# Kernel tuning notes

Hardware: AMD Instinct MI355X
Metric: run time of the kernel (lower is better)

## Reference

```python
import jax, jax.numpy as jnp
import numpy as np

MIN_C = 1e-6
MIN_NORM = 1e-15
BALL_EPS = 0.004  # float32 ball epsilon


def _norm(x):
    return jnp.maximum(jnp.linalg.norm(x, axis=-1, keepdims=True), MIN_NORM)


def _project(x, c):
    norm = _norm(x)
    maxnorm = (1.0 - BALL_EPS) / jnp.sqrt(c)
    return jnp.where(norm > maxnorm, x / norm * maxnorm, x)


def _tanh(x):
    return jnp.tanh(jnp.clip(x, -15.0, 15.0))


def _artanh(x):
    x = jnp.clip(x, -1.0 + 1e-5, 1.0 - 1e-5)
    return 0.5 * (jnp.log1p(x) - jnp.log1p(-x))


def _expmap0(u, c):
    sc = jnp.sqrt(c)
    n = _norm(u)
    return _project(_tanh(sc * n) * u / (sc * n), c)


def _logmap0(y, c):
    sc = jnp.sqrt(c)
    n = _norm(y)
    return y / n / sc * _artanh(sc * n)


def _mobius_add(x, y, c):
    x2 = jnp.sum(x * x, -1, keepdims=True)
    y2 = jnp.sum(y * y, -1, keepdims=True)
    xy = jnp.sum(x * y, -1, keepdims=True)
    num = (1 + 2 * c * xy + c * y2) * x + (1 - c * x2) * y
    den = jnp.maximum(1 + 2 * c * xy + c * c * x2 * y2, MIN_NORM)
    return num / den


N_NODE, N_EDGE, D, ATTN, B, N_VOCAB = 100000, 1000000, 64, 64, 256, 401


def setup_inputs() -> dict:
    key = jax.random.key(0)
    ks = jax.random.split(key, 12)
    r_idx = jax.random.randint(ks[0], (N_EDGE,), 0, B, dtype=jnp.int32)
    rel = jax.random.randint(ks[1], (N_EDGE,), 0, N_VOCAB, dtype=jnp.int32)
    sub = jax.random.randint(ks[2], (N_EDGE,), 0, N_NODE, dtype=jnp.int32)
    obj = jax.random.randint(ks[3], (N_EDGE,), 0, N_NODE, dtype=jnp.int32)
    zero = jnp.zeros((N_EDGE,), jnp.int32)
    edges = jnp.stack([r_idx, zero, rel, zero, sub, obj], axis=1)  # [E, 6]
    s = 0.1
    return {
        "hidden": jax.random.normal(ks[4], (N_NODE, D), jnp.float32) * s,
        "q_rel": jax.random.randint(ks[5], (B,), 0, N_VOCAB, dtype=jnp.int32),
        "edges": edges,
        "rela_embed": jax.random.normal(ks[6], (N_VOCAB, D), jnp.float32) * s,
        "Ws_w": jax.random.normal(ks[7], (ATTN, D), jnp.float32) * s,
        "Wr_w": jax.random.normal(ks[8], (ATTN, D), jnp.float32) * s,
        "Wqr_w": jax.random.normal(ks[9], (ATTN, D), jnp.float32) * s,
        "Wqr_b": jnp.zeros((ATTN,), jnp.float32),
        "Wattn_w": jax.random.normal(ks[10], (1, ATTN), jnp.float32) * s,
        "Wh_w": jax.random.normal(ks[11], (D, D), jnp.float32) * s,
        "n_node": N_NODE,
    }


def reference(hidden, q_rel, edges, rela_embed, Ws_w, Wr_w, Wqr_w, Wqr_b, Wattn_w, Wh_w, n_node):
    c = MIN_C
    sub, rel, obj, r_idx = edges[:, 4], edges[:, 2], edges[:, 5], edges[:, 0]
    hs = hidden[sub]                 # [E, D] gather
    hr = rela_embed[rel]             # [E, D]
    h_qr = rela_embed[q_rel][r_idx]  # [E, D]
    # attention MLP -> scalar gate per edge
    pre = hs @ Ws_w.T + hr @ Wr_w.T + h_qr @ Wqr_w.T + Wqr_b
    alpha = jax.nn.sigmoid(jax.nn.relu(pre) @ Wattn_w.T)  # [E, 1]
    # hyperbolic message
    hs_h = _expmap0(hs, c)
    hr_h = _expmap0(hr, c)
    mess2 = _logmap0(_project(_mobius_add(hs_h, hr_h, c), c), c)
    message = mess2 * alpha
    agg = jax.ops.segment_sum(message, obj, num_segments=n_node)  # scatter-add
    a = _expmap0(agg @ Wh_w.T, c)
    a = jax.nn.relu(a)  # act
    return _logmap0(a, c)
```

## Files before the change

### kernel.cpp

```cpp
#include <hip/hip_runtime.h>
#include <math.h>
#include <stdint.h>

#define N_NODE 100000
#define N_EDGE 1000000
#define DIM    64
#define NB     256
#define NVOCAB 401
#define AGG_WAVES 8192
#define NSTREAM (AGG_WAVES * 4)

#define BSH    9
#define BMSK   511
#define NBKT   ((N_NODE + BMSK) >> BSH)
#define CHKE   1024
#define NCHK   ((N_EDGE + CHKE - 1) / CHKE)
#define SCAN_TOT (NBKT * NCHK)
#define SCANA_GRID ((SCAN_TOT + 1023) / 1024)

typedef short short8  __attribute__((ext_vector_type(8)));
typedef float floatx4 __attribute__((ext_vector_type(4)));
typedef unsigned short ushort_t;

__device__ inline unsigned short f2bf_rne(float f)
{
    unsigned u = __float_as_uint(f);
    unsigned r = u + 0x7FFF + ((u >> 16) & 1);
    return (unsigned short)(r >> 16);
}
__device__ inline float bflo(unsigned u) { return __uint_as_float(u << 16); }
__device__ inline float bfhi(unsigned u) { return __uint_as_float(u & 0xFFFF0000u); }
__device__ inline unsigned short f2h(float f)
{
    _Float16 h = (_Float16)f;
    unsigned short s; __builtin_memcpy(&s, &h, 2); return s;
}
__device__ inline float h2f(unsigned b)
{
    unsigned short s = (unsigned short)b;
    _Float16 h; __builtin_memcpy(&h, &s, 2); return (float)h;
}

__device__ inline void split8(float4 v0, float4 v1, short8& hi, short8& lo)
{
    float f[8] = {v0.x, v0.y, v0.z, v0.w, v1.x, v1.y, v1.z, v1.w};
    #pragma unroll
    for (int j = 0; j < 8; ++j) {
        unsigned u = __float_as_uint(f[j]);
        unsigned r = u + 0x7FFF + ((u >> 16) & 1);
        unsigned short h = (unsigned short)(r >> 16);
        float hf = __uint_as_float(((unsigned)h) << 16);
        float l  = f[j] - hf;
        unsigned u2 = __float_as_uint(l);
        unsigned r2 = u2 + 0x7FFF + ((u2 >> 16) & 1);
        hi[j] = (short)h;
        lo[j] = (short)(r2 >> 16);
    }
}

#define INIT_GRID ((4 * 4096 + 255) / 256)

__global__ __launch_bounds__(256) void init_kernel(
    const float* __restrict__ Ws, const float* __restrict__ Wr,
    const float* __restrict__ Wqr, const float* __restrict__ Wh,
    ushort_t* __restrict__ wsp)
{
    int tid = blockIdx.x * 256 + threadIdx.x;
    if (tid < 4 * 4096) {
        int w = tid >> 12, e = tid & 4095;
        const float* src = (w == 0) ? Ws : (w == 1) ? Wr : (w == 2) ? Wqr : Wh;
        float f = src[e];
        unsigned u = __float_as_uint(f);
        unsigned r = u + 0x7FFF + ((u >> 16) & 1);
        unsigned short h = (unsigned short)(r >> 16);
        float hf = __uint_as_float(((unsigned)h) << 16);
        float l  = f - hf;
        unsigned u2 = __float_as_uint(l);
        unsigned r2 = u2 + 0x7FFF + ((u2 >> 16) & 1);
        wsp[w * 8192 + e]        = h;
        wsp[w * 8192 + 4096 + e] = (unsigned short)(r2 >> 16);
    }
}

__device__ void gemm64p_body(
    const float* __restrict__ X,
    const int*   __restrict__ idx,
    const ushort_t* __restrict__ Whi,
    const ushort_t* __restrict__ Wlo,
    const float* __restrict__ bias,
    void* __restrict__ Yv,
    ushort_t* __restrict__ Y2,
    int R, int out_mode, int blk)
{
    int wave = threadIdx.x >> 6;
    int lane = threadIdx.x & 63;
    int m    = lane & 15;
    int quad = lane >> 4;
    int r0   = blk * 64 + wave * 16;

    int r = r0 + m;
    int src = (r < R) ? (idx ? idx[r] : r) : 0;
    const float* xrow = X + (size_t)src * DIM + quad * 8;

    float4 a0[2], a1[2];
    #pragma unroll
    for (int c = 0; c < 2; ++c) {
        a0[c] = *(const float4*)(xrow + 32 * c);
        a1[c] = *(const float4*)(xrow + 32 * c + 4);
    }
    short8 ah[2], al[2];
    #pragma unroll
    for (int c = 0; c < 2; ++c) split8(a0[c], a1[c], ah[c], al[c]);

    if (out_mode == 3 && r < R) {
        #pragma unroll
        for (int c = 0; c < 2; ++c)
            *(short8*)(Y2 + (size_t)r * DIM + 32 * c + quad * 8) = ah[c];
    }

    floatx4 acc[4] = {{0,0,0,0},{0,0,0,0},{0,0,0,0},{0,0,0,0}};
    #pragma unroll
    for (int g = 0; g < 4; ++g) {
        const ushort_t* whrow = Whi + (size_t)(g * 16 + m) * DIM + quad * 8;
        const ushort_t* wlrow = Wlo + (size_t)(g * 16 + m) * DIM + quad * 8;
        #pragma unroll
        for (int c = 0; c < 2; ++c) {
            short8 bh = *(const short8*)(whrow + 32 * c);
            short8 bl = *(const short8*)(wlrow + 32 * c);
            acc[g] = __builtin_amdgcn_mfma_f32_16x16x32_bf16(bh, ah[c], acc[g], 0, 0, 0);
            acc[g] = __builtin_amdgcn_mfma_f32_16x16x32_bf16(bl, ah[c], acc[g], 0, 0, 0);
            acc[g] = __builtin_amdgcn_mfma_f32_16x16x32_bf16(bh, al[c], acc[g], 0, 0, 0);
        }
    }

    if (r < R) {
        #pragma unroll
        for (int g = 0; g < 4; ++g) {
            float4 bv = make_float4(0.f, 0.f, 0.f, 0.f);
            if (bias) bv = *(const float4*)(bias + g * 16 + quad * 4);
            float v0 = acc[g][0] + bv.x;
            float v1 = acc[g][1] + bv.y;
            float v2 = acc[g][2] + bv.z;
            float v3 = acc[g][3] + bv.w;
            if (out_mode == 1) {
                v0 = fmaxf(v0, 0.f); v1 = fmaxf(v1, 0.f);
                v2 = fmaxf(v2, 0.f); v3 = fmaxf(v3, 0.f);
            }
            if (out_mode >= 2) {
                uint2 o;
                o.x = (unsigned)f2bf_rne(v0) | ((unsigned)f2bf_rne(v1) << 16);
                o.y = (unsigned)f2bf_rne(v2) | ((unsigned)f2bf_rne(v3) << 16);
                *(uint2*)((ushort_t*)Yv + (size_t)r * DIM + g * 16 + quad * 4) = o;
            } else {
                *(float4*)((float*)Yv + (size_t)r * DIM + g * 16 + quad * 4) =
                    make_float4(v0, v1, v2, v3);
            }
        }
    }
}

__global__ __launch_bounds__(256) void gemm64p_bf16A_kernel(
    const ushort_t* __restrict__ A,
    const ushort_t* __restrict__ Whi,
    const ushort_t* __restrict__ Wlo,
    float* __restrict__ Y, int R)
{
    int wave = threadIdx.x >> 6;
    int lane = threadIdx.x & 63;
    int m    = lane & 15;
    int quad = lane >> 4;
    int r0   = blockIdx.x * 64 + wave * 16;

    int r = r0 + m;
    int src = (r < R) ? r : 0;
    short8 a8[2];
    #pragma unroll
    for (int c = 0; c < 2; ++c)
        a8[c] = *(const short8*)(A + (size_t)src * DIM + 32 * c + quad * 8);

    floatx4 acc[4] = {{0,0,0,0},{0,0,0,0},{0,0,0,0},{0,0,0,0}};
    #pragma unroll
    for (int g = 0; g < 4; ++g) {
        const ushort_t* whrow = Whi + (size_t)(g * 16 + m) * DIM + quad * 8;
        const ushort_t* wlrow = Wlo + (size_t)(g * 16 + m) * DIM + quad * 8;
        #pragma unroll
        for (int c = 0; c < 2; ++c) {
            short8 bh = *(const short8*)(whrow + 32 * c);
            short8 bl = *(const short8*)(wlrow + 32 * c);
            acc[g] = __builtin_amdgcn_mfma_f32_16x16x32_bf16(bh, a8[c], acc[g], 0, 0, 0);
            acc[g] = __builtin_amdgcn_mfma_f32_16x16x32_bf16(bl, a8[c], acc[g], 0, 0, 0);
        }
    }

    if (r < R) {
        #pragma unroll
        for (int g = 0; g < 4; ++g) {
            *(float4*)(Y + (size_t)r * DIM + g * 16 + quad * 4) =
                make_float4(fmaxf(acc[g][0], 0.f), fmaxf(acc[g][1], 0.f),
                            fmaxf(acc[g][2], 0.f), fmaxf(acc[g][3], 0.f));
        }
    }
}

__device__ void gemm64_body(
    const float* __restrict__ X,
    const int*   __restrict__ idx,
    const float* __restrict__ W,
    const float* __restrict__ bias,
    void* __restrict__ Yv,
    ushort_t* __restrict__ Y2,
    int R, int out_mode, int blk)
{
    int wave = threadIdx.x >> 6;
    int lane = threadIdx.x & 63;
    int m    = lane & 15;
    int quad = lane >> 4;
    int r0   = blk * 64 + wave * 16;

    int r = r0 + m;
    int src = (r < R) ? (idx ? idx[r] : r) : 0;
    const float* xrow = X + (size_t)src * DIM + quad * 8;

    float4 a0[2], a1[2];
    #pragma unroll
    for (int c = 0; c < 2; ++c) {
        a0[c] = *(const float4*)(xrow + 32 * c);
        a1[c] = *(const float4*)(xrow + 32 * c + 4);
    }
    short8 ah[2], al[2];
    #pragma unroll
    for (int c = 0; c < 2; ++c) split8(a0[c], a1[c], ah[c], al[c]);

    if (out_mode == 3 && r < R) {
        #pragma unroll
        for (int c = 0; c < 2; ++c)
            *(short8*)(Y2 + (size_t)r * DIM + 32 * c + quad * 8) = ah[c];
    }

    floatx4 acc[4] = {{0,0,0,0},{0,0,0,0},{0,0,0,0},{0,0,0,0}};
    #pragma unroll
    for (int g = 0; g < 4; ++g) {
        const float* wrow = W + (size_t)(g * 16 + m) * DIM + quad * 8;
        #pragma unroll
        for (int c = 0; c < 2; ++c) {
            float4 b0 = *(const float4*)(wrow + 32 * c);
            float4 b1 = *(const float4*)(wrow + 32 * c + 4);
            short8 bh, bl;
            split8(b0, b1, bh, bl);
            acc[g] = __builtin_amdgcn_mfma_f32_16x16x32_bf16(ah[c], bh, acc[g], 0, 0, 0);
            acc[g] = __builtin_amdgcn_mfma_f32_16x16x32_bf16(ah[c], bl, acc[g], 0, 0, 0);
            acc[g] = __builtin_amdgcn_mfma_f32_16x16x32_bf16(al[c], bh, acc[g], 0, 0, 0);
        }
    }

    #pragma unroll
    for (int g = 0; g < 4; ++g) {
        float bv = bias ? bias[g * 16 + m] : 0.0f;
        #pragma unroll
        for (int reg = 0; reg < 4; ++reg) {
            int rr = r0 + quad * 4 + reg;
            if (rr < R) {
                float v = acc[g][reg] + bv;
                if (out_mode == 1) v = fmaxf(v, 0.0f);
                if (out_mode >= 2)
                    ((ushort_t*)Yv)[(size_t)rr * DIM + g * 16 + m] = f2bf_rne(v);
                else
                    ((float*)Yv)[(size_t)rr * DIM + g * 16 + m] = v;
            }
        }
    }
}

__global__ __launch_bounds__(256) void gemm64_kernel(
    const float* __restrict__ X, const int* __restrict__ idx,
    const float* __restrict__ W, const float* __restrict__ bias,
    void* __restrict__ Yv, ushort_t* __restrict__ Y2, int R, int out_mode)
{
    gemm64_body(X, idx, W, bias, Yv, Y2, R, out_mode, blockIdx.x);
}

#define G1 ((N_NODE + 63) / 64)
#define G2 ((NVOCAB + 63) / 64)
#define G3 (NB / 64)
#define GSMALL (G2 + G3)
#define PREPC_GRID (NCHK + GSMALL + G1)

__global__ __launch_bounds__(256) void prepcount_kernel(
    const float* __restrict__ hidden,
    const float* __restrict__ rela,
    const int*   __restrict__ q_rel,
    const ushort_t* __restrict__ wsp,
    const float* __restrict__ Wqr_b,
    ushort_t* __restrict__ hsWs,
    ushort_t* __restrict__ hidb,
    ushort_t* __restrict__ rel_preb,
    ushort_t* __restrict__ relab,
    ushort_t* __restrict__ qr_preb,
    const int* __restrict__ edges,
    int2* __restrict__ epack,
    int* __restrict__ histBB)
{
    int b = blockIdx.x;
    if (b < NCHK) {
        __shared__ unsigned cnt[NBKT];
        if (threadIdx.x < NBKT) cnt[threadIdx.x] = 0;
        __syncthreads();
        int base = b * CHKE + threadIdx.x;
        #pragma unroll
        for (int k = 0; k < 4; ++k) {
            int e = base + k * 256;
            if (e < N_EDGE) {
                int2 ab = *(const int2*)(edges + (size_t)e * 6);
                int2 cd = *(const int2*)(edges + (size_t)e * 6 + 2);
                int2 ef = *(const int2*)(edges + (size_t)e * 6 + 4);
                epack[e] = make_int2(ef.x | (cd.x << 17), ef.y | (ab.x << 17));
                atomicAdd(&cnt[ef.y >> BSH], 1u);
            }
        }
        __syncthreads();
        if (threadIdx.x < NBKT)
            histBB[b * NBKT + threadIdx.x] = (int)cnt[threadIdx.x];
    } else if (b < NCHK + G2) {
        gemm64p_body(rela, nullptr, wsp + 1 * 8192, wsp + 1 * 8192 + 4096,
                     nullptr, rel_preb, relab, NVOCAB, 3, b - NCHK);
    } else if (b < NCHK + GSMALL) {
        gemm64p_body(rela, q_rel, wsp + 2 * 8192, wsp + 2 * 8192 + 4096,
                     Wqr_b, qr_preb, nullptr, NB, 2, b - NCHK - G2);
    } else {
        gemm64p_body(hidden, nullptr, wsp, wsp + 4096,
                     nullptr, hsWs, hidb, N_NODE, 3, b - NCHK - GSMALL);
    }
}

__global__ __launch_bounds__(1024) void scanA_kernel(
    const int* __restrict__ histBB, int* __restrict__ offs2,
    int* __restrict__ partialA)
{
    __shared__ int s[1024];
    int t = threadIdx.x;
    int m = blockIdx.x * 1024 + t;
    int v = 0;
    if (m < SCAN_TOT) {
        int bin = m / NCHK, ch = m - bin * NCHK;
        v = histBB[ch * NBKT + bin];
    }
    s[t] = v;
    __syncthreads();
    for (int off = 1; off < 1024; off <<= 1) {
        int add = (t >= off) ? s[t - off] : 0;
        __syncthreads();
        s[t] += add;
        __syncthreads();
    }
    if (m < SCAN_TOT) offs2[m] = s[t] - v;
    if (t == 1023) partialA[blockIdx.x] = s[1023];
}

__global__ __launch_bounds__(1024) void scanC_kernel(
    int* __restrict__ offs2, const int* __restrict__ partialA,
    int* __restrict__ bstart)
{
    __shared__ int s[1024];
    __shared__ int pbase_s;
    int t = threadIdx.x;
    int pb = (t < (int)blockIdx.x) ? partialA[t] : 0;
    s[t] = pb;
    __syncthreads();
    for (int off = 1024 / 2; off; off >>= 1) {
        if (t < off) s[t] += s[t + off];
        __syncthreads();
    }
    if (t == 0) pbase_s = s[0];
    __syncthreads();
    int pbase = pbase_s;

    int m = blockIdx.x * 1024 + t;
    if (m < SCAN_TOT) {
        int val = offs2[m] + pbase;
        offs2[m] = val;
        int bin = m / NCHK, ch = m - bin * NCHK;
        if (ch == 0) bstart[bin] = val;
    }
    if (blockIdx.x == 0 && t == 0) bstart[NBKT] = N_EDGE;
}

__global__ __launch_bounds__(1024) void alpha_scatter_kernel(
    const int2*     __restrict__ epack,
    const int*      __restrict__ offs2,
    const ushort_t* __restrict__ hsWs,
    const ushort_t* __restrict__ rel_preb,
    const ushort_t* __restrict__ qr_preb,
    const float*    __restrict__ wattn,
    int2*           __restrict__ csr2)
{
    __shared__ int offL[NBKT];
    int blk = blockIdx.x;
    if (threadIdx.x < NBKT)
        offL[threadIdx.x] = offs2[threadIdx.x * NCHK + blk];
    __syncthreads();

    int wave = threadIdx.x >> 6;
    int lane = threadIdx.x & 63;
    int q    = lane >> 4;
    int l    = lane & 15;
    int f0   = l * 4;
    float4 wa = *(const float4*)(wattn + f0);

    #pragma unroll
    for (int it = 0; it < 4; ++it) {
        int e0 = blk * CHKE + wave * 64 + it * 16 + q * 4;

        int   sub[4], rl[4], ob[4];
        float tt[4];
        #pragma unroll
        for (int j = 0; j < 4; ++j) {
            int e = e0 + j;
            int2 ep = epack[min(e, N_EDGE - 1)];
            sub[j] = ep.x & 0x1FFFF;
            rl[j]  = (int)((unsigned)ep.x >> 17);
            ob[j]  = ep.y & 0x1FFFF;
            int ri = (int)((unsigned)ep.y >> 17);

            uint2 uh = *(const uint2*)(hsWs     + (((unsigned)sub[j]) << 6) + f0);
            uint2 ur = *(const uint2*)(rel_preb + (((unsigned)rl[j])  << 6) + f0);
            uint2 uq = *(const uint2*)(qr_preb  + (((unsigned)ri)     << 6) + f0);

            float s0 =  fmaxf(bflo(uh.x) + bflo(ur.x) + bflo(uq.x), 0.f) * wa.x;
            s0 = fmaf(fmaxf(bfhi(uh.x) + bfhi(ur.x) + bfhi(uq.x), 0.f), wa.y, s0);
            s0 = fmaf(fmaxf(bflo(uh.y) + bflo(ur.y) + bflo(uq.y), 0.f), wa.z, s0);
            s0 = fmaf(fmaxf(bfhi(uh.y) + bfhi(ur.y) + bfhi(uq.y), 0.f), wa.w, s0);
            tt[j] = s0;
        }
        #pragma unroll
        for (int j = 0; j < 4; ++j) {
            tt[j] += __shfl_xor(tt[j], 1);
            tt[j] += __shfl_xor(tt[j], 2);
            tt[j] += __shfl_xor(tt[j], 4);
            tt[j] += __shfl_xor(tt[j], 8);
        }

        if (l < 4) {
            int j = l;
            int e = e0 + j;
            if (e < N_EDGE) {
                float alpha = 1.0f / (1.0f + __expf(-tt[j]));
                int bin  = ob[j] >> BSH;
                int slot = atomicAdd(&offL[bin], 1);
                csr2[slot] = make_int2(sub[j] | ((ob[j] & BMSK) << 17),
                    (int)(((unsigned)rl[j] << 16) | f2h(alpha)));
            }
        }
    }
}

__global__ __launch_bounds__(512) void node_sort_kernel(
    const int2* __restrict__ csr2,
    const int*  __restrict__ bstart,
    int2* __restrict__ csr3,
    int*  __restrict__ offs)
{
    __shared__ int cnt[512], incl[512];
    int b = blockIdx.x;
    int start = bstart[b];
    int end   = bstart[b + 1];
    int len   = end - start;

    cnt[threadIdx.x] = 0;
    __syncthreads();
    for (int t = threadIdx.x; t < len; t += 512) {
        unsigned x = (unsigned)csr2[start + t].x;
        atomicAdd(&cnt[x >> 17], 1);
    }
    __syncthreads();
    incl[threadIdx.x] = cnt[threadIdx.x];
    __syncthreads();
    for (int off = 1; off < 512; off <<= 1) {
        int add = ((int)threadIdx.x >= off) ? incl[threadIdx.x - off] : 0;
        __syncthreads();
        incl[threadIdx.x] += add;
        __syncthreads();
    }
    {
        int excl = incl[threadIdx.x] - cnt[threadIdx.x];
        int n = (b << BSH) + threadIdx.x;
        if (n < N_NODE) offs[n] = start + excl;
        cnt[threadIdx.x] = excl;
    }
    if (b == 0 && threadIdx.x == 0) offs[N_NODE] = N_EDGE;
    if (b == 0 && threadIdx.x < 32) csr3[N_EDGE + threadIdx.x] = make_int2(0, 0);
    __syncthreads();
    for (int t = threadIdx.x; t < len; t += 512) {
        int2 ed = csr2[start + t];
        int row = (int)((unsigned)ed.x >> 17);
        int pos = start + atomicAdd(&cnt[row], 1);
        csr3[pos] = ed;
    }
}

__global__ __launch_bounds__(256) void agg_kernel(
    const int2*     __restrict__ csr3,
    const int*      __restrict__ offs,
    const ushort_t* __restrict__ hB,
    const ushort_t* __restrict__ relab,
    ushort_t* __restrict__ aggb)
{
    int l  = threadIdx.x & 15;
    int f0 = l * 4;
    int n  = (blockIdx.x * 256 + threadIdx.x) >> 4;

    int i   = offs[n];
    int end = offs[n + 1];
    while (n < N_NODE) {
        int nn = n + NSTREAM;
        int ni = 0, ne = 0;
        if (nn < N_NODE) { ni = offs[nn]; ne = offs[nn + 1]; }

        float4 acc = make_float4(0.f, 0.f, 0.f, 0.f);
        int2 e[4];
        #pragma unroll
        for (int j = 0; j < 4; ++j) e[j] = csr3[i + j];
        while (i < end) {
            int2 p[4];
            #pragma unroll
            for (int j = 0; j < 4; ++j) p[j] = csr3[i + 4 + j];

            uint2 uh[4], ur[4];
            #pragma unroll
            for (int j = 0; j < 4; ++j) {
                unsigned ex = (unsigned)e[j].x, ey = (unsigned)e[j].y;
                uh[j] = *(const uint2*)(hB    + ((ex & 0x1FFFFu) << 6) + f0);
                ur[j] = *(const uint2*)(relab + ((ey >> 16) << 6) + f0);
            }
            #pragma unroll
            for (int j = 0; j < 4; ++j) {
                unsigned ey = (unsigned)e[j].y;
                float v  = (i + j < end) ? 1.0f : 0.0f;
                float al = v * h2f(ey & 0xFFFFu);
                acc.x = fmaf(al, bflo(uh[j].x) + bflo(ur[j].x), acc.x);
                acc.y = fmaf(al, bfhi(uh[j].x) + bfhi(ur[j].x), acc.y);
                acc.z = fmaf(al, bflo(uh[j].y) + bflo(ur[j].y), acc.z);
                acc.w = fmaf(al, bfhi(uh[j].y) + bfhi(ur[j].y), acc.w);
            }
            #pragma unroll
            for (int j = 0; j < 4; ++j) e[j] = p[j];
            i += 4;
        }

        uint2 o;
        o.x = (unsigned)f2bf_rne(acc.x) | ((unsigned)f2bf_rne(acc.y) << 16);
        o.y = (unsigned)f2bf_rne(acc.z) | ((unsigned)f2bf_rne(acc.w) << 16);
        *(uint2*)(aggb + (((unsigned)n) << 6) + f0) = o;

        n = nn; i = ni; end = ne;
    }
}

__global__ __launch_bounds__(256) void edge_kernel(
    const int*      __restrict__ edges,
    const ushort_t* __restrict__ hB,
    const ushort_t* __restrict__ relab,
    const ushort_t* __restrict__ hsWs,
    const ushort_t* __restrict__ rel_preb,
    const ushort_t* __restrict__ qr_preb,
    const float*    __restrict__ wattn,
    float* __restrict__ out)
{
    int e = (blockIdx.x * blockDim.x + threadIdx.x) >> 6;
    if (e >= N_EDGE) return;
    int lane = threadIdx.x & 63;
    int r_i = edges[e * 6 + 0];
    int rl  = edges[e * 6 + 2];
    int sb  = edges[e * 6 + 4];
    int ob  = edges[e * 6 + 5];
    float hs = __uint_as_float(((unsigned)hB[(size_t)sb * DIM + lane]) << 16);
    float hr = __uint_as_float(((unsigned)relab[(size_t)rl * DIM + lane]) << 16);
    float p1 = __uint_as_float(((unsigned)hsWs[(size_t)sb * DIM + lane]) << 16);
    float p2 = __uint_as_float(((unsigned)rel_preb[(size_t)rl * DIM + lane]) << 16);
    float p3 = __uint_as_float(((unsigned)qr_preb[(size_t)r_i * DIM + lane]) << 16);
    float t = wattn[lane] * fmaxf(p1 + p2 + p3, 0.0f);
    #pragma unroll
    for (int off = 32; off; off >>= 1) t += __shfl_xor(t, off);
    float alpha = 1.0f / (1.0f + __expf(-t));
    atomicAdd(&out[(size_t)ob * DIM + lane], (hs + hr) * alpha);
}

extern "C" void kernel_launch(void* const* d_in, const int* in_sizes, int n_in,
                              void* d_out, int out_size, void* d_ws, size_t ws_size,
                              hipStream_t stream)
{
    const float* hidden = (const float*)d_in[0];
    const int*   q_rel  = (const int*)  d_in[1];
    const int*   edges  = (const int*)  d_in[2];
    const float* rela   = (const float*)d_in[3];
    const float* Ws     = (const float*)d_in[4];
    const float* Wr     = (const float*)d_in[5];
    const float* Wqr    = (const float*)d_in[6];
    const float* Wqr_b  = (const float*)d_in[7];
    const float* Wattn  = (const float*)d_in[8];
    const float* Wh     = (const float*)d_in[9];
    float* out = (float*)d_out;

    ushort_t* qr_preb  = (ushort_t*)d_ws;
    ushort_t* rel_preb = qr_preb + NB * DIM;
    ushort_t* relab    = rel_preb + NVOCAB * DIM;
    ushort_t* hsWs     = relab + NVOCAB * DIM;
    ushort_t* hidb     = hsWs + (size_t)N_NODE * DIM;
    int2* epack  = (int2*)(((uintptr_t)(hidb + (size_t)N_NODE * DIM) + 15) & ~(uintptr_t)15);
    int*  histBB = (int*)(epack + N_EDGE);
    int*  offs2  = histBB + SCAN_TOT;
    int*  partialA = offs2 + SCAN_TOT;
    int*  bstart   = partialA + 1024;
    int2* csr2   = (int2*)(((uintptr_t)(bstart + NBKT + 1) + 15) & ~(uintptr_t)15);
    ushort_t* wsp = (ushort_t*)(csr2 + N_EDGE);
    int2* csr3   = (int2*)(wsp + 4 * 8192);
    int*  offs   = (int*)(csr3 + N_EDGE + 32);
    size_t csr_need = ((char*)(offs + N_NODE + 1)) - (char*)d_ws;
    bool use_csr = ws_size >= csr_need;
    ushort_t* aggb = (ushort_t*)epack;

    if (use_csr) {
        init_kernel<<<INIT_GRID, 256, 0, stream>>>(Ws, Wr, Wqr, Wh, wsp);
        prepcount_kernel<<<PREPC_GRID, 256, 0, stream>>>(
            hidden, rela, q_rel, wsp, Wqr_b,
            hsWs, hidb, rel_preb, relab, qr_preb, edges, epack, histBB);
        scanA_kernel<<<SCANA_GRID, 1024, 0, stream>>>(histBB, offs2, partialA);
        scanC_kernel<<<SCANA_GRID, 1024, 0, stream>>>(offs2, partialA, bstart);
        alpha_scatter_kernel<<<NCHK, 1024, 0, stream>>>(
            epack, offs2, hsWs, rel_preb, qr_preb, Wattn, csr2);
        node_sort_kernel<<<NBKT, 512, 0, stream>>>(csr2, bstart, csr3, offs);
        agg_kernel<<<AGG_WAVES / 4, 256, 0, stream>>>(csr3, offs, hidb, relab, aggb);
        gemm64p_bf16A_kernel<<<(N_NODE + 63) / 64, 256, 0, stream>>>(
            aggb, wsp + 3 * 8192, wsp + 3 * 8192 + 4096, out, N_NODE);
    } else {
        gemm64_kernel<<<(NVOCAB + 63) / 64, 256, 0, stream>>>(
            rela, nullptr, Wr, nullptr, rel_preb, relab, NVOCAB, 3);
        gemm64_kernel<<<(NB + 63) / 64, 256, 0, stream>>>(
            rela, q_rel, Wqr, Wqr_b, qr_preb, nullptr, NB, 2);
        gemm64_kernel<<<(N_NODE + 63) / 64, 256, 0, stream>>>(
            hidden, nullptr, Ws, nullptr, hsWs, hidb, N_NODE, 3);
        hipMemsetAsync(d_out, 0, (size_t)N_NODE * DIM * sizeof(float), stream);
        edge_kernel<<<(N_EDGE + 3) / 4, 256, 0, stream>>>(
            edges, hidb, relab, hsWs, rel_preb, qr_preb, Wattn, out);
        gemm64_kernel<<<(N_NODE + 63) / 64, 256, 0, stream>>>(
            out, nullptr, Wh, nullptr, out, nullptr, N_NODE, 1);
    }
}
```

Baseline: 230.6 us.

## Fuse attention gate into aggregation and interleave hsWs/hidden rows

Moves the per-edge attention-logit and sigmoid computation out of the scatter kernel into the CSR aggregation kernel. The scatter pass becomes a plain index shuffle that packs rel and query-relation indices. The node projection now writes one interleaved 128-element bf16 row per node (Ws-projected and raw hidden features in alternating 4-element blocks), so each edge needs one 16-byte gather instead of two separate row reads. The cost is an extra random pass over hsWs-derived data in scatter removed, in exchange for more gathers (rel_preb, qr_preb) and shuffle reductions inside the aggregation loop.

```diff
diff --git a/kernel.cpp b/kernel.cpp
--- a/kernel.cpp
+++ b/kernel.cpp
@@ -30,16 +30,7 @@
 }
 __device__ inline float bflo(unsigned u) { return __uint_as_float(u << 16); }
 __device__ inline float bfhi(unsigned u) { return __uint_as_float(u & 0xFFFF0000u); }
-__device__ inline unsigned short f2h(float f)
-{
-    _Float16 h = (_Float16)f;
-    unsigned short s; __builtin_memcpy(&s, &h, 2); return s;
-}
-__device__ inline float h2f(unsigned b)
-{
-    unsigned short s = (unsigned short)b;
-    _Float16 h; __builtin_memcpy(&h, &s, 2); return (float)h;
-}
+__device__ inline unsigned us16(short s) { return (unsigned)(unsigned short)s; }
 
 __device__ inline void split8(float4 v0, float4 v1, short8& hi, short8& lo)
 {
@@ -117,6 +108,20 @@
         for (int c = 0; c < 2; ++c)
             *(short8*)(Y2 + (size_t)r * DIM + 32 * c + quad * 8) = ah[c];
     }
+    if (out_mode == 4 && r < R) {
+        ushort_t* hhrow = (ushort_t*)Yv + (size_t)r * 128;
+        #pragma unroll
+        for (int c = 0; c < 2; ++c) {
+            int fb = quad * 2 + 8 * c;
+            uint2 o1, o2;
+            o1.x = us16(ah[c][0]) | (us16(ah[c][1]) << 16);
+            o1.y = us16(ah[c][2]) | (us16(ah[c][3]) << 16);
+            o2.x = us16(ah[c][4]) | (us16(ah[c][5]) << 16);
+            o2.y = us16(ah[c][6]) | (us16(ah[c][7]) << 16);
+            *(uint2*)(hhrow + fb * 8 + 4)       = o1;
+            *(uint2*)(hhrow + (fb + 1) * 8 + 4) = o2;
+        }
+    }
 
     floatx4 acc[4] = {{0,0,0,0},{0,0,0,0},{0,0,0,0},{0,0,0,0}};
     #pragma unroll
@@ -146,7 +151,14 @@
                 v0 = fmaxf(v0, 0.f); v1 = fmaxf(v1, 0.f);
                 v2 = fmaxf(v2, 0.f); v3 = fmaxf(v3, 0.f);
             }
-            if (out_mode >= 2) {
+            if (out_mode == 4) {
+                ushort_t* hhrow = (ushort_t*)Yv + (size_t)r * 128;
+                int fblk = g * 4 + quad;
+                uint2 o;
+                o.x = (unsigned)f2bf_rne(v0) | ((unsigned)f2bf_rne(v1) << 16);
+                o.y = (unsigned)f2bf_rne(v2) | ((unsigned)f2bf_rne(v3) << 16);
+                *(uint2*)(hhrow + fblk * 8) = o;
+            } else if (out_mode >= 2) {
                 uint2 o;
                 o.x = (unsigned)f2bf_rne(v0) | ((unsigned)f2bf_rne(v1) << 16);
                 o.y = (unsigned)f2bf_rne(v2) | ((unsigned)f2bf_rne(v3) << 16);
@@ -291,8 +303,7 @@
     const int*   __restrict__ q_rel,
     const ushort_t* __restrict__ wsp,
     const float* __restrict__ Wqr_b,
-    ushort_t* __restrict__ hsWs,
-    ushort_t* __restrict__ hidb,
+    ushort_t* __restrict__ hh,
     ushort_t* __restrict__ rel_preb,
     ushort_t* __restrict__ relab,
     ushort_t* __restrict__ qr_preb,
@@ -328,7 +339,7 @@
                      Wqr_b, qr_preb, nullptr, NB, 2, b - NCHK - G2);
     } else {
         gemm64p_body(hidden, nullptr, wsp, wsp + 4096,
-                     nullptr, hsWs, hidb, N_NODE, 3, b - NCHK - GSMALL);
+                     nullptr, hh, nullptr, N_NODE, 4, b - NCHK - GSMALL);
     }
 }
 
@@ -384,71 +395,28 @@
     if (blockIdx.x == 0 && t == 0) bstart[NBKT] = N_EDGE;
 }
 
-__global__ __launch_bounds__(1024) void alpha_scatter_kernel(
-    const int2*     __restrict__ epack,
-    const int*      __restrict__ offs2,
-    const ushort_t* __restrict__ hsWs,
-    const ushort_t* __restrict__ rel_preb,
-    const ushort_t* __restrict__ qr_preb,
-    const float*    __restrict__ wattn,
-    int2*           __restrict__ csr2)
+__global__ __launch_bounds__(256) void scatter_kernel(
+    const int2* __restrict__ epack,
+    const int*  __restrict__ offs2,
+    int2*       __restrict__ csr2)
 {
     __shared__ int offL[NBKT];
     int blk = blockIdx.x;
     if (threadIdx.x < NBKT)
         offL[threadIdx.x] = offs2[threadIdx.x * NCHK + blk];
     __syncthreads();
-
-    int wave = threadIdx.x >> 6;
-    int lane = threadIdx.x & 63;
-    int q    = lane >> 4;
-    int l    = lane & 15;
-    int f0   = l * 4;
-    float4 wa = *(const float4*)(wattn + f0);
-
-    #pragma unroll
-    for (int it = 0; it < 4; ++it) {
-        int e0 = blk * CHKE + wave * 64 + it * 16 + q * 4;
-
-        int   sub[4], rl[4], ob[4];
-        float tt[4];
-        #pragma unroll
-        for (int j = 0; j < 4; ++j) {
-            int e = e0 + j;
-            int2 ep = epack[min(e, N_EDGE - 1)];
-            sub[j] = ep.x & 0x1FFFF;
-            rl[j]  = (int)((unsigned)ep.x >> 17);
-            ob[j]  = ep.y & 0x1FFFF;
-            int ri = (int)((unsigned)ep.y >> 17);
-
-            uint2 uh = *(const uint2*)(hsWs     + (((unsigned)sub[j]) << 6) + f0);
-            uint2 ur = *(const uint2*)(rel_preb + (((unsigned)rl[j])  << 6) + f0);
-            uint2 uq = *(const uint2*)(qr_preb  + (((unsigned)ri)     << 6) + f0);
-
-            float s0 =  fmaxf(bflo(uh.x) + bflo(ur.x) + bflo(uq.x), 0.f) * wa.x;
-            s0 = fmaf(fmaxf(bfhi(uh.x) + bfhi(ur.x) + bfhi(uq.x), 0.f), wa.y, s0);
-            s0 = fmaf(fmaxf(bflo(uh.y) + bflo(ur.y) + bflo(uq.y), 0.f), wa.z, s0);
-            s0 = fmaf(fmaxf(bfhi(uh.y) + bfhi(ur.y) + bfhi(uq.y), 0.f), wa.w, s0);
-            tt[j] = s0;
-        }
-        #pragma unroll
-        for (int j = 0; j < 4; ++j) {
-            tt[j] += __shfl_xor(tt[j], 1);
-            tt[j] += __shfl_xor(tt[j], 2);
-            tt[j] += __shfl_xor(tt[j], 4);
-            tt[j] += __shfl_xor(tt[j], 8);
-        }
-
-        if (l < 4) {
-            int j = l;
-            int e = e0 + j;
-            if (e < N_EDGE) {
-                float alpha = 1.0f / (1.0f + __expf(-tt[j]));
-                int bin  = ob[j] >> BSH;
-                int slot = atomicAdd(&offL[bin], 1);
-                csr2[slot] = make_int2(sub[j] | ((ob[j] & BMSK) << 17),
-                    (int)(((unsigned)rl[j] << 16) | f2h(alpha)));
-            }
+    int base = blk * CHKE + threadIdx.x;
+    #pragma unroll
+    for (int k = 0; k < 4; ++k) {
+        int e = base + k * 256;
+        if (e < N_EDGE) {
+            int2 ep = epack[e];
+            int sub = ep.x & 0x1FFFF;
+            int rl  = (int)((unsigned)ep.x >> 17);
+            int ob  = ep.y & 0x1FFFF;
+            int ri  = (int)((unsigned)ep.y >> 17);
+            int slot = atomicAdd(&offL[ob >> BSH], 1);
+            csr2[slot] = make_int2(sub | ((ob & BMSK) << 17), rl | (ri << 9));
         }
     }
 }
@@ -500,13 +468,18 @@
 __global__ __launch_bounds__(256) void agg_kernel(
     const int2*     __restrict__ csr3,
     const int*      __restrict__ offs,
-    const ushort_t* __restrict__ hB,
+    const ushort_t* __restrict__ hh,
+    const ushort_t* __restrict__ rel_preb,
+    const ushort_t* __restrict__ qr_preb,
     const ushort_t* __restrict__ relab,
+    const float*    __restrict__ wattn,
     ushort_t* __restrict__ aggb)
 {
     int l  = threadIdx.x & 15;
     int f0 = l * 4;
     int n  = (blockIdx.x * 256 + threadIdx.x) >> 4;
+
+    float4 wa = *(const float4*)(wattn + f0);
 
     int i   = offs[n];
     int end = offs[n + 1];
@@ -524,22 +497,35 @@
             #pragma unroll
             for (int j = 0; j < 4; ++j) p[j] = csr3[i + 4 + j];
 
-            uint2 uh[4], ur[4];
+            uint4 hv[4];
+            uint2 up[4], uq[4], ua[4];
             #pragma unroll
             for (int j = 0; j < 4; ++j) {
                 unsigned ex = (unsigned)e[j].x, ey = (unsigned)e[j].y;
-                uh[j] = *(const uint2*)(hB    + ((ex & 0x1FFFFu) << 6) + f0);
-                ur[j] = *(const uint2*)(relab + ((ey >> 16) << 6) + f0);
+                unsigned sub = ex & 0x1FFFFu;
+                unsigned rl  = ey & 0x1FFu;
+                unsigned ri  = (ey >> 9) & 0xFFu;
+                hv[j] = *(const uint4*)(hh + (sub << 7) + l * 8);
+                up[j] = *(const uint2*)(rel_preb + (rl << 6) + f0);
+                uq[j] = *(const uint2*)(qr_preb  + (ri << 6) + f0);
+                ua[j] = *(const uint2*)(relab    + (rl << 6) + f0);
             }
             #pragma unroll
             for (int j = 0; j < 4; ++j) {
-                unsigned ey = (unsigned)e[j].y;
+                float t =  fmaxf(bflo(hv[j].x) + bflo(up[j].x) + bflo(uq[j].x), 0.f) * wa.x;
+                t = fmaf(fmaxf(bfhi(hv[j].x) + bfhi(up[j].x) + bfhi(uq[j].x), 0.f), wa.y, t);
+                t = fmaf(fmaxf(bflo(hv[j].y) + bflo(up[j].y) + bflo(uq[j].y), 0.f), wa.z, t);
+                t = fmaf(fmaxf(bfhi(hv[j].y) + bfhi(up[j].y) + bfhi(uq[j].y), 0.f), wa.w, t);
+                t += __shfl_xor(t, 1);
+                t += __shfl_xor(t, 2);
+                t += __shfl_xor(t, 4);
+                t += __shfl_xor(t, 8);
                 float v  = (i + j < end) ? 1.0f : 0.0f;
-                float al = v * h2f(ey & 0xFFFFu);
-                acc.x = fmaf(al, bflo(uh[j].x) + bflo(ur[j].x), acc.x);
-                acc.y = fmaf(al, bfhi(uh[j].x) + bfhi(ur[j].x), acc.y);
-                acc.z = fmaf(al, bflo(uh[j].y) + bflo(ur[j].y), acc.z);
-                acc.w = fmaf(al, bfhi(uh[j].y) + bfhi(ur[j].y), acc.w);
+                float al = v / (1.0f + __expf(-t));
+                acc.x = fmaf(al, bflo(hv[j].z) + bflo(ua[j].x), acc.x);
+                acc.y = fmaf(al, bfhi(hv[j].z) + bfhi(ua[j].x), acc.y);
+                acc.z = fmaf(al, bflo(hv[j].w) + bflo(ua[j].y), acc.z);
+                acc.w = fmaf(al, bfhi(hv[j].w) + bfhi(ua[j].y), acc.w);
             }
             #pragma unroll
             for (int j = 0; j < 4; ++j) e[j] = p[j];
@@ -603,9 +589,8 @@
     ushort_t* qr_preb  = (ushort_t*)d_ws;
     ushort_t* rel_preb = qr_preb + NB * DIM;
     ushort_t* relab    = rel_preb + NVOCAB * DIM;
-    ushort_t* hsWs     = relab + NVOCAB * DIM;
-    ushort_t* hidb     = hsWs + (size_t)N_NODE * DIM;
-    int2* epack  = (int2*)(((uintptr_t)(hidb + (size_t)N_NODE * DIM) + 15) & ~(uintptr_t)15);
+    ushort_t* hh       = relab + NVOCAB * DIM;
+    int2* epack  = (int2*)(((uintptr_t)(hh + (size_t)N_NODE * 128) + 15) & ~(uintptr_t)15);
     int*  histBB = (int*)(epack + N_EDGE);
     int*  offs2  = histBB + SCAN_TOT;
     int*  partialA = offs2 + SCAN_TOT;
@@ -622,25 +607,27 @@
         init_kernel<<<INIT_GRID, 256, 0, stream>>>(Ws, Wr, Wqr, Wh, wsp);
         prepcount_kernel<<<PREPC_GRID, 256, 0, stream>>>(
             hidden, rela, q_rel, wsp, Wqr_b,
-            hsWs, hidb, rel_preb, relab, qr_preb, edges, epack, histBB);
+            hh, rel_preb, relab, qr_preb, edges, epack, histBB);
         scanA_kernel<<<SCANA_GRID, 1024, 0, stream>>>(histBB, offs2, partialA);
         scanC_kernel<<<SCANA_GRID, 1024, 0, stream>>>(offs2, partialA, bstart);
-        alpha_scatter_kernel<<<NCHK, 1024, 0, stream>>>(
-            epack, offs2, hsWs, rel_preb, qr_preb, Wattn, csr2);
+        scatter_kernel<<<NCHK, 256, 0, stream>>>(epack, offs2, csr2);
         node_sort_kernel<<<NBKT, 512, 0, stream>>>(csr2, bstart, csr3, offs);
-        agg_kernel<<<AGG_WAVES / 4, 256, 0, stream>>>(csr3, offs, hidb, relab, aggb);
+        agg_kernel<<<AGG_WAVES / 4, 256, 0, stream>>>(
+            csr3, offs, hh, rel_preb, qr_preb, relab, Wattn, aggb);
         gemm64p_bf16A_kernel<<<(N_NODE + 63) / 64, 256, 0, stream>>>(
             aggb, wsp + 3 * 8192, wsp + 3 * 8192 + 4096, out, N_NODE);
     } else {
+        ushort_t* hsWs_fb = hh;
+        ushort_t* hidb_fb = hh + (size_t)N_NODE * DIM;
         gemm64_kernel<<<(NVOCAB + 63) / 64, 256, 0, stream>>>(
             rela, nullptr, Wr, nullptr, rel_preb, relab, NVOCAB, 3);
         gemm64_kernel<<<(NB + 63) / 64, 256, 0, stream>>>(
             rela, q_rel, Wqr, Wqr_b, qr_preb, nullptr, NB, 2);
         gemm64_kernel<<<(N_NODE + 63) / 64, 256, 0, stream>>>(
-            hidden, nullptr, Ws, nullptr, hsWs, hidb, N_NODE, 3);
+            hidden, nullptr, Ws, nullptr, hsWs_fb, hidb_fb, N_NODE, 3);
         hipMemsetAsync(d_out, 0, (size_t)N_NODE * DIM * sizeof(float), stream);
         edge_kernel<<<(N_EDGE + 3) / 4, 256, 0, stream>>>(
-            edges, hidb, relab, hsWs, rel_preb, qr_preb, Wattn, out);
+            edges, hidb_fb, relab, hsWs_fb, rel_preb, qr_preb, Wattn, out);
         gemm64_kernel<<<(N_NODE + 63) / 64, 256, 0, stream>>>(
             out, nullptr, Wh, nullptr, out, nullptr, N_NODE, 1);
     }
```

New measurement: 234.3 us. No clear change (+1.6%).
